# Kernel optimization log

Hardware: AMD Instinct MI355X
Metric: run time of the kernel (lower is better)

## Reference

```python
import jax, jax.numpy as jnp
import numpy as np

N_S = 4096      # number of sentences
N_K = 8192      # number of knowledge entries
HID = 1024      # settings.hidden_dim
SENT = 1024     # settings.sent_dim


def setup_inputs() -> dict:
    key = jax.random.key(0)
    ks = jax.random.split(key, 6)
    sentences = jax.random.normal(ks[0], (N_S, SENT), dtype=jnp.float32)
    knowledge = jax.random.normal(ks[1], (N_K, 3 * HID), dtype=jnp.float32)
    # Linear params stored as [in, out] for x @ W + b
    Ws = jax.random.normal(ks[2], (SENT, HID), dtype=jnp.float32) * 0.02
    bs = jnp.zeros((HID,), dtype=jnp.float32)
    Wk = jax.random.normal(ks[3], (3 * HID, HID), dtype=jnp.float32) * 0.02
    bk = jnp.zeros((HID,), dtype=jnp.float32)
    return {"sentences": sentences, "knowledge": knowledge,
            "Ws": Ws, "bs": bs, "Wk": Wk, "bk": bk}


def reference(sentences, knowledge, Ws, bs, Wk, bk):
    S = sentences @ Ws + bs                  # [N_s, h]
    K = knowledge @ Wk + bk                  # [N_k, h]
    align_scores = S @ K.T                   # [N_s, N_k]
    # NOTE: softmax over dim=0 (sentence axis), exactly as the torch module
    attentions = jax.nn.softmax(align_scores, axis=0)
    fused = attentions @ knowledge           # [N_s, 3h]
    return (fused, attentions)
```

## Files before the change

### kernel.cpp

```cpp
#include <hip/hip_runtime.h>
#include <hip/hip_bf16.h>
#include <cstdint>
#include <cstddef>

#define N_S 4096
#define N_Kn 8192
#define HID 1024
#define SENT 1024
#define K3 3072

typedef __attribute__((ext_vector_type(4))) float f4;
typedef __attribute__((ext_vector_type(8))) short bf8;
typedef __attribute__((ext_vector_type(4))) short bf4;
typedef unsigned short u16;

__device__ __forceinline__ u16 f2bf(float x) {
    __hip_bfloat16 h = __float2bfloat16(x);
    return __builtin_bit_cast(u16, h);
}
__device__ __forceinline__ float bf2f(u16 u) {
    union { unsigned int u; float f; } v; v.u = ((unsigned int)u) << 16;
    return v.f;
}

__device__ __forceinline__ void gl16(const u16* g, u16* l) {
    __builtin_amdgcn_global_load_lds(
        (const __attribute__((address_space(1))) void*)g,
        (__attribute__((address_space(3))) void*)l, 16, 0, 0);
}

__device__ __forceinline__ int xcd_swz(int bid, int nwg) {
    const int cpx = nwg >> 3;
    return (bid & 7) * cpx + (bid >> 3);
}

__global__ __launch_bounds__(256) void transpose_split_f32(
    const float* __restrict__ in, u16* __restrict__ hi, u16* __restrict__ lo,
    int R, int C)
{
    __shared__ float tile[32][33];
    const int bx = blockIdx.x * 32, by = blockIdx.y * 32;
    const int tx = threadIdx.x & 31, ty = threadIdx.x >> 5;
#pragma unroll
    for (int i = 0; i < 32; i += 8)
        tile[ty + i][tx] = in[(size_t)(by + ty + i) * C + bx + tx];
    __syncthreads();
#pragma unroll
    for (int i = 0; i < 32; i += 8) {
        const float v = tile[tx][ty + i];
        const u16 h = f2bf(v);
        const size_t o = (size_t)(bx + ty + i) * R + by + tx;
        hi[o] = h;
        lo[o] = f2bf(v - bf2f(h));
    }
}

__global__ __launch_bounds__(256) void transpose_f32_bf16(
    const float* __restrict__ in, u16* __restrict__ out, int R, int C)
{
    __shared__ float tile[32][33];
    const int bx = blockIdx.x * 32, by = blockIdx.y * 32;
    const int tx = threadIdx.x & 31, ty = threadIdx.x >> 5;
#pragma unroll
    for (int i = 0; i < 32; i += 8)
        tile[ty + i][tx] = in[(size_t)(by + ty + i) * C + bx + tx];
    __syncthreads();
#pragma unroll
    for (int i = 0; i < 32; i += 8)
        out[(size_t)(bx + ty + i) * R + by + tx] = f2bf(tile[tx][ty + i]);
}

#define G8_LDA(buf, mh) \
  _Pragma("unroll") for (int m_ = 0; m_ < 4; ++m_) \
  _Pragma("unroll") for (int kk_ = 0; kk_ < 2; ++kk_) \
    fa[m_][kk_] = *(const bf8*)&sA[buf][wm][((mh)*64 + m_*16 + fr)*64 + (((kk_*4+kg) ^ (fr&7))<<3)];

#define G8_LDB(buf, nh, FB) \
  _Pragma("unroll") for (int nn_ = 0; nn_ < 2; ++nn_) \
  _Pragma("unroll") for (int kk_ = 0; kk_ < 2; ++kk_) \
    FB[nn_][kk_] = *(const bf8*)&sB[buf][hb][(cb + (nh)*32 + nn_*16 + fr)*64 + (((kk_*4+kg) ^ (fr&7))<<3)];

#define G8_MMA(mh, nh, FB) \
  _Pragma("unroll") for (int kk_ = 0; kk_ < 2; ++kk_) \
  _Pragma("unroll") for (int m_ = 0; m_ < 4; ++m_) \
  _Pragma("unroll") for (int nn_ = 0; nn_ < 2; ++nn_) \
    acc[(mh)*4+m_][(nh)*2+nn_] = __builtin_amdgcn_mfma_f32_16x16x32_bf16( \
        fa[m_][kk_], FB[nn_][kk_], acc[(mh)*4+m_][(nh)*2+nn_], 0, 0, 0);

#define BARR __builtin_amdgcn_s_barrier()
#define PRIO1 __builtin_amdgcn_s_setprio(1)
#define PRIO0 __builtin_amdgcn_s_setprio(0)
#define VM8  asm volatile("s_waitcnt vmcnt(8)" ::: "memory")
#define VM0  asm volatile("s_waitcnt vmcnt(0)" ::: "memory")

__global__ __launch_bounds__(512, 2) void gemm8(
    const u16* __restrict__ A, const u16* __restrict__ B,
    float* __restrict__ C, int N, int Kd, int gx)
{
    __shared__ u16 sA[2][2][8192];
    __shared__ u16 sB[2][2][8192];

    const int swz = xcd_swz(blockIdx.x, gridDim.x);
    const int bx = swz % gx, by = swz / gx;
    const long brow = (long)by * 256, bcol = (long)bx * 256;

    const int t = threadIdx.x;
    const int w = t >> 6, l = t & 63;
    const int fr = l & 15, kg = l >> 4;
    const int wm = w >> 2;
    const int wn = w & 3;
    const int hb = wn >> 1;
    const int cb = (wn & 1) * 64;

    const int srow = t >> 3;
    const int schk = ((t & 7) ^ (srow & 7)) << 3;
    const int sldb = w << 9;

    auto stA = [&](int buf, int h, int kt) {
        const u16* g = A + (brow + h * 128 + srow) * (long)Kd + ((long)kt << 6) + schk;
        gl16(g, &sA[buf][h][sldb]);
        gl16(g + 64 * (long)Kd, &sA[buf][h][4096 + sldb]);
    };
    auto stB = [&](int buf, int h, int kt) {
        const u16* g = B + (bcol + h * 128 + srow) * (long)Kd + ((long)kt << 6) + schk;
        gl16(g, &sB[buf][h][sldb]);
        gl16(g + 64 * (long)Kd, &sB[buf][h][4096 + sldb]);
    };

    f4 acc[8][4];
#pragma unroll
    for (int m = 0; m < 8; ++m)
#pragma unroll
        for (int n = 0; n < 4; ++n) acc[m][n] = (f4){0.f, 0.f, 0.f, 0.f};

    bf8 fa[4][2], fb0[2][2], fb1[2][2];

    const int NK = Kd >> 6;

    stB(0, 0, 0); stB(0, 1, 0); stA(0, 0, 0); stA(0, 1, 0);
    stB(1, 0, 1); stB(1, 1, 1); stA(1, 0, 1); stA(1, 1, 1);
    VM8;
    BARR;

    for (int it = 0; it < (NK >> 1); ++it) {
        const int t2 = 2 * it + 2, t3 = 2 * it + 3;
        const bool s2 = t2 < NK, s3 = t3 < NK;

        G8_LDA(0, 0); G8_LDB(0, 0, fb0);
        BARR; PRIO1; G8_MMA(0, 0, fb0); PRIO0; BARR;
        G8_LDB(0, 1, fb1);
        BARR; PRIO1; G8_MMA(0, 1, fb1); PRIO0; BARR;
        G8_LDA(0, 1);
        if (s2) { stB(0, 0, t2); stB(0, 1, t2); }
        BARR; PRIO1; G8_MMA(1, 0, fb0); PRIO0; BARR;
        if (s2) { stA(0, 0, t2); stA(0, 1, t2); }
        BARR; PRIO1; G8_MMA(1, 1, fb1); PRIO0;
        if (s2) { VM8; } else { VM0; }
        BARR;

        G8_LDA(1, 0); G8_LDB(1, 0, fb0);
        BARR; PRIO1; G8_MMA(0, 0, fb0); PRIO0; BARR;
        G8_LDB(1, 1, fb1);
        BARR; PRIO1; G8_MMA(0, 1, fb1); PRIO0; BARR;
        G8_LDA(1, 1);
        if (s3) { stB(1, 0, t3); stB(1, 1, t3); }
        BARR; PRIO1; G8_MMA(1, 0, fb0); PRIO0; BARR;
        if (s3) { stA(1, 0, t3); stA(1, 1, t3); }
        BARR; PRIO1; G8_MMA(1, 1, fb1); PRIO0;
        if (s3) { VM8; } else { VM0; }
        BARR;
    }

#pragma unroll
    for (int n = 0; n < 4; ++n) {
        const long c = bcol + wn * 64 + n * 16 + fr;
#pragma unroll
        for (int m = 0; m < 8; ++m) {
            const long r0 = brow + wm * 128 + m * 16 + kg * 4;
#pragma unroll
            for (int r = 0; r < 4; ++r)
                C[(r0 + r) * (long)N + c] = acc[m][n][r];
        }
    }
}

template <bool SPLIT, bool AF32, bool EPIS>
__global__ __launch_bounds__(256) void gemm_mfma(
    const void* __restrict__ Aany, const u16* __restrict__ Alo_,
    const u16* __restrict__ Bhi_, const u16* __restrict__ Blo_,
    float* __restrict__ Cf, u16* __restrict__ Chi, u16* __restrict__ Clo,
    const float* __restrict__ bias, int N, int Kd, int gx)
{
    constexpr int SA = AF32 ? 48 : 32;
    __shared__ u16 sAh[128 * SA];
    __shared__ u16 sAl[SPLIT ? 128 * SA : 8];
    __shared__ u16 sBh[128 * 32];
    __shared__ u16 sBl[SPLIT ? 128 * 32 : 8];

    const int swz = xcd_swz(blockIdx.x, gridDim.x);
    const int nst_x = gx >> 2;
    const int st = swz >> 4, off = swz & 15;
    const int bxi = (st % nst_x) * 4 + (off & 3);
    const int byi = (st / nst_x) * 4 + (off >> 2);

    const int t = threadIdx.x;
    const int w = t >> 6;
    const int l = t & 63;
    const long brow = (long)byi * 128;
    const long bcol = (long)bxi * 128;

    const int grow = l >> 2;
    const int gcol = ((l & 3) ^ ((l >> 3) & 3)) * 8;

    const int wr = (w >> 1) * 64;
    const int wc = (w & 1) * 64;
    const int fr = l & 15;
    const int kg = l >> 4;
    const int kq = (kg ^ ((fr >> 1) & 3)) * 8;

    f4 acc[4][4];
#pragma unroll
    for (int m = 0; m < 4; m++)
#pragma unroll
        for (int n = 0; n < 4; n++) acc[m][n] = (f4){0.f, 0.f, 0.f, 0.f};

    const int nkt = Kd >> 5;
    for (int kt = 0; kt < nkt; ++kt) {
        const int k0 = kt * 32;

#pragma unroll
        for (int i = 0; i < 2; ++i) {
            const long r = bcol + i * 64 + w * 16 + grow;
            const int lb = i * 2048 + w * 512;
            gl16(Bhi_ + r * Kd + k0 + gcol, sBh + lb);
            if constexpr (SPLIT) gl16(Blo_ + r * Kd + k0 + gcol, sBl + lb);
        }

        if constexpr (!AF32) {
            const u16* Ahi = (const u16*)Aany;
#pragma unroll
            for (int i = 0; i < 2; ++i) {
                const long r = brow + i * 64 + w * 16 + grow;
                const int lb = i * 2048 + w * 512;
                gl16(Ahi + r * Kd + k0 + gcol, sAh + lb);
                if constexpr (SPLIT) gl16(Alo_ + r * Kd + k0 + gcol, sAl + lb);
            }
        } else {
            const float* Af = (const float*)Aany;
            const int ar = w * 8 + (l >> 3);
            const int cF = (l & 7) * 4;
#pragma unroll
            for (int j = 0; j < 4; ++j) {
                const int r = j * 32 + ar;
                const f4 v = *(const f4*)(Af + (brow + r) * (long)Kd + k0 + cF);
                u16 h[4], lw[4];
#pragma unroll
                for (int q = 0; q < 4; ++q) {
                    h[q] = f2bf(v[q]);
                    if constexpr (SPLIT) lw[q] = f2bf(v[q] - bf2f(h[q]));
                }
                *(bf4*)&sAh[r * SA + cF] = *(bf4*)h;
                if constexpr (SPLIT) *(bf4*)&sAl[r * SA + cF] = *(bf4*)lw;
            }
        }
        __syncthreads();

        bf8 fah[4], fbh[4], fal[4], fbl[4];
#pragma unroll
        for (int m = 0; m < 4; ++m) {
            if constexpr (AF32) {
                fah[m] = *(bf8*)&sAh[(wr + m * 16 + fr) * SA + kg * 8];
                if constexpr (SPLIT) fal[m] = *(bf8*)&sAl[(wr + m * 16 + fr) * SA + kg * 8];
            } else {
                fah[m] = *(bf8*)&sAh[(wr + m * 16 + fr) * 32 + kq];
                if constexpr (SPLIT) fal[m] = *(bf8*)&sAl[(wr + m * 16 + fr) * 32 + kq];
            }
            fbh[m] = *(bf8*)&sBh[(wc + m * 16 + fr) * 32 + kq];
            if constexpr (SPLIT) fbl[m] = *(bf8*)&sBl[(wc + m * 16 + fr) * 32 + kq];
        }
#pragma unroll
        for (int m = 0; m < 4; ++m)
#pragma unroll
            for (int n = 0; n < 4; ++n) {
                acc[m][n] = __builtin_amdgcn_mfma_f32_16x16x32_bf16(fah[m], fbh[n], acc[m][n], 0, 0, 0);
                if constexpr (SPLIT) {
                    acc[m][n] = __builtin_amdgcn_mfma_f32_16x16x32_bf16(fah[m], fbl[n], acc[m][n], 0, 0, 0);
                    acc[m][n] = __builtin_amdgcn_mfma_f32_16x16x32_bf16(fal[m], fbh[n], acc[m][n], 0, 0, 0);
                }
            }
        __syncthreads();
    }

#pragma unroll
    for (int n = 0; n < 4; ++n) {
        const long c = bcol + wc + n * 16 + fr;
        float bv = 0.f;
        if constexpr (EPIS) bv = bias[c];
#pragma unroll
        for (int m = 0; m < 4; ++m) {
            const long r0 = brow + wr + m * 16 + kg * 4;
#pragma unroll
            for (int r = 0; r < 4; ++r) {
                const float v = acc[m][n][r] + bv;
                if constexpr (EPIS) {
                    const u16 h = f2bf(v);
                    Chi[(r0 + r) * (long)N + c] = h;
                    Clo[(r0 + r) * (long)N + c] = f2bf(v - bf2f(h));
                } else {
                    Cf[(r0 + r) * (long)N + c] = v;
                }
            }
        }
    }
}

#define RCHUNK 128

__global__ __launch_bounds__(256) void softmax_partial(
    const float* __restrict__ align, float* __restrict__ pm, float* __restrict__ ps)
{
    const int col = blockIdx.x * 256 + threadIdx.x;
    const int r0 = blockIdx.y * RCHUNK;
    float m = -3.4e38f;
    for (int r = 0; r < RCHUNK; r++)
        m = fmaxf(m, align[(size_t)(r0 + r) * N_Kn + col]);
    float s = 0.f;
    for (int r = 0; r < RCHUNK; r++)
        s += __expf(align[(size_t)(r0 + r) * N_Kn + col] - m);
    pm[(size_t)blockIdx.y * N_Kn + col] = m;
    ps[(size_t)blockIdx.y * N_Kn + col] = s;
}

__global__ __launch_bounds__(256) void softmax_combine(
    const float* __restrict__ pm, const float* __restrict__ ps,
    float* __restrict__ fm, float* __restrict__ fsinv)
{
    const int col = blockIdx.x * 256 + threadIdx.x;
    float m = -3.4e38f;
#pragma unroll
    for (int i = 0; i < 32; i++) m = fmaxf(m, pm[(size_t)i * N_Kn + col]);
    float s = 0.f;
#pragma unroll
    for (int i = 0; i < 32; i++)
        s += ps[(size_t)i * N_Kn + col] * __expf(pm[(size_t)i * N_Kn + col] - m);
    fm[col] = m;
    fsinv[col] = 1.f / s;
}

__global__ __launch_bounds__(256) void softmax_norm(
    float* __restrict__ align, u16* __restrict__ abf,
    const float* __restrict__ fm, const float* __restrict__ fsinv)
{
    const int col = blockIdx.x * 256 + threadIdx.x;
    const int r0 = blockIdx.y * RCHUNK;
    const float m = fm[col], si = fsinv[col];
    for (int r = 0; r < RCHUNK; r++) {
        const size_t idx = (size_t)(r0 + r) * N_Kn + col;
        const float v = __expf(align[idx] - m) * si;
        align[idx] = v;
        abf[idx] = f2bf(v);
    }
}

extern "C" void kernel_launch(void* const* d_in, const int* in_sizes, int n_in,
                              void* d_out, int out_size, void* d_ws, size_t ws_size,
                              hipStream_t stream)
{
    const float* sentences = (const float*)d_in[0];
    const float* knowledge = (const float*)d_in[1];
    const float* Ws = (const float*)d_in[2];
    const float* bs = (const float*)d_in[3];
    const float* Wk = (const float*)d_in[4];
    const float* bk = (const float*)d_in[5];

    float* out_fused = (float*)d_out;
    float* out_attn = (float*)d_out + (size_t)N_S * K3;

    char* w = (char*)d_ws;
    u16* attn_bf = (u16*)w;
    u16* WsT_hi = (u16*)w; w += (size_t)HID * SENT * 2;
    u16* WsT_lo = (u16*)w; w += (size_t)HID * SENT * 2;
    u16* WkT_hi = (u16*)w; w += (size_t)HID * K3 * 2;
    u16* WkT_lo = (u16*)w; w += (size_t)HID * K3 * 2;
    u16* S_hi   = (u16*)w; w += (size_t)N_S * HID * 2;
    u16* S_lo   = (u16*)w; w += (size_t)N_S * HID * 2;
    u16* K_hi   = (u16*)w; w += (size_t)N_Kn * HID * 2;
    u16* K_lo   = (u16*)w; w += (size_t)N_Kn * HID * 2;
    u16* kT     = (u16*)w; w += (size_t)K3 * N_Kn * 2;
    float* pm   = (float*)w; w += (size_t)32 * N_Kn * 4;
    float* ps   = (float*)w; w += (size_t)32 * N_Kn * 4;
    float* fm   = (float*)w; w += (size_t)N_Kn * 4;
    float* fsv  = (float*)w; w += (size_t)N_Kn * 4;

    transpose_split_f32<<<dim3(HID / 32, SENT / 32), 256, 0, stream>>>(Ws, WsT_hi, WsT_lo, SENT, HID);
    transpose_split_f32<<<dim3(HID / 32, K3 / 32), 256, 0, stream>>>(Wk, WkT_hi, WkT_lo, K3, HID);
    transpose_f32_bf16<<<dim3(K3 / 32, N_Kn / 32), 256, 0, stream>>>(knowledge, kT, N_Kn, K3);

    gemm_mfma<true, true, true><<<(HID / 128) * (N_S / 128), 256, 0, stream>>>(
        sentences, nullptr, WsT_hi, WsT_lo, nullptr, S_hi, S_lo, bs, HID, SENT, HID / 128);

    gemm_mfma<true, true, true><<<(HID / 128) * (N_Kn / 128), 256, 0, stream>>>(
        knowledge, nullptr, WkT_hi, WkT_lo, nullptr, K_hi, K_lo, bk, HID, K3, HID / 128);

    gemm_mfma<true, false, false><<<(N_Kn / 128) * (N_S / 128), 256, 0, stream>>>(
        S_hi, S_lo, K_hi, K_lo, out_attn, nullptr, nullptr, nullptr, N_Kn, HID, N_Kn / 128);

    softmax_partial<<<dim3(N_Kn / 256, N_S / RCHUNK), 256, 0, stream>>>(out_attn, pm, ps);
    softmax_combine<<<dim3(N_Kn / 256), 256, 0, stream>>>(pm, ps, fm, fsv);
    softmax_norm<<<dim3(N_Kn / 256, N_S / RCHUNK), 256, 0, stream>>>(out_attn, attn_bf, fm, fsv);

    gemm8<<<(K3 / 256) * (N_S / 256), 512, 0, stream>>>(
        attn_bf, kT, out_fused, K3, N_Kn, K3 / 256);
}
```

Baseline: 783.5 us.

## Retile final attention-knowledge GEMM to 256x192 blocks for full CU occupancy

Replaces the 256x256-tile GEMM for attn @ knowledge with a 256x192-tile variant using a 4x2 wave layout of 64x96 sub-tiles and a single-step double-buffered K loop with prefetched B fragments. The grid grows from 192 to 256 blocks, which should fill all compute units instead of leaving some idle. In exchange, per-block data reuse is lower and the pipeline schedule and wait counts are rewritten, so there is a risk of less latency hiding.

```diff
diff --git a/kernel.cpp b/kernel.cpp
--- a/kernel.cpp
+++ b/kernel.cpp
@@ -70,113 +70,106 @@
         out[(size_t)(bx + ty + i) * R + by + tx] = f2bf(tile[tx][ty + i]);
 }
 
-#define G8_LDA(buf, mh) \
-  _Pragma("unroll") for (int m_ = 0; m_ < 4; ++m_) \
-  _Pragma("unroll") for (int kk_ = 0; kk_ < 2; ++kk_) \
-    fa[m_][kk_] = *(const bf8*)&sA[buf][wm][((mh)*64 + m_*16 + fr)*64 + (((kk_*4+kg) ^ (fr&7))<<3)];
-
-#define G8_LDB(buf, nh, FB) \
-  _Pragma("unroll") for (int nn_ = 0; nn_ < 2; ++nn_) \
-  _Pragma("unroll") for (int kk_ = 0; kk_ < 2; ++kk_) \
-    FB[nn_][kk_] = *(const bf8*)&sB[buf][hb][(cb + (nh)*32 + nn_*16 + fr)*64 + (((kk_*4+kg) ^ (fr&7))<<3)];
-
-#define G8_MMA(mh, nh, FB) \
-  _Pragma("unroll") for (int kk_ = 0; kk_ < 2; ++kk_) \
-  _Pragma("unroll") for (int m_ = 0; m_ < 4; ++m_) \
-  _Pragma("unroll") for (int nn_ = 0; nn_ < 2; ++nn_) \
-    acc[(mh)*4+m_][(nh)*2+nn_] = __builtin_amdgcn_mfma_f32_16x16x32_bf16( \
-        fa[m_][kk_], FB[nn_][kk_], acc[(mh)*4+m_][(nh)*2+nn_], 0, 0, 0);
-
 #define BARR __builtin_amdgcn_s_barrier()
 #define PRIO1 __builtin_amdgcn_s_setprio(1)
 #define PRIO0 __builtin_amdgcn_s_setprio(0)
-#define VM8  asm volatile("s_waitcnt vmcnt(8)" ::: "memory")
+#define VM7  asm volatile("s_waitcnt vmcnt(7)" ::: "memory")
 #define VM0  asm volatile("s_waitcnt vmcnt(0)" ::: "memory")
 
-__global__ __launch_bounds__(512, 2) void gemm8(
+#define GB_LDA(buf, mh) \
+  _Pragma("unroll") for (int mf_ = 0; mf_ < 2; ++mf_) \
+  _Pragma("unroll") for (int kk_ = 0; kk_ < 2; ++kk_) \
+    fa[mf_][kk_] = *(const bf8*)&sA[buf][(wm*64 + ((mh)*2+mf_)*16 + fr)*64 + (((kk_*4+kg) ^ (fr&7))<<3)];
+
+#define GB_LDB(buf, nh, FB) \
+  _Pragma("unroll") for (int nf_ = 0; nf_ < 3; ++nf_) \
+  _Pragma("unroll") for (int kk_ = 0; kk_ < 2; ++kk_) \
+    FB[nf_][kk_] = *(const bf8*)&sB[buf][(wn*96 + ((nh)*3+nf_)*16 + fr)*64 + (((kk_*4+kg) ^ (fr&7))<<3)];
+
+#define GB_MMA(mh, nh, FB) \
+  _Pragma("unroll") for (int kk_ = 0; kk_ < 2; ++kk_) \
+  _Pragma("unroll") for (int mf_ = 0; mf_ < 2; ++mf_) \
+  _Pragma("unroll") for (int nf_ = 0; nf_ < 3; ++nf_) \
+    acc[(mh)*2+mf_][(nh)*3+nf_] = __builtin_amdgcn_mfma_f32_16x16x32_bf16( \
+        fa[mf_][kk_], FB[nf_][kk_], acc[(mh)*2+mf_][(nh)*3+nf_], 0, 0, 0);
+
+__global__ __launch_bounds__(512, 2) void gemm8b(
     const u16* __restrict__ A, const u16* __restrict__ B,
     float* __restrict__ C, int N, int Kd, int gx)
 {
-    __shared__ u16 sA[2][2][8192];
-    __shared__ u16 sB[2][2][8192];
+    __shared__ u16 sA[2][256 * 64];
+    __shared__ u16 sB[2][192 * 64];
 
     const int swz = xcd_swz(blockIdx.x, gridDim.x);
     const int bx = swz % gx, by = swz / gx;
-    const long brow = (long)by * 256, bcol = (long)bx * 256;
+    const long brow = (long)by * 256, bcol = (long)bx * 192;
 
     const int t = threadIdx.x;
     const int w = t >> 6, l = t & 63;
     const int fr = l & 15, kg = l >> 4;
-    const int wm = w >> 2;
-    const int wn = w & 3;
-    const int hb = wn >> 1;
-    const int cb = (wn & 1) * 64;
+    const int wm = w >> 1;
+    const int wn = w & 1;
 
     const int srow = t >> 3;
     const int schk = ((t & 7) ^ (srow & 7)) << 3;
     const int sldb = w << 9;
 
-    auto stA = [&](int buf, int h, int kt) {
-        const u16* g = A + (brow + h * 128 + srow) * (long)Kd + ((long)kt << 6) + schk;
-        gl16(g, &sA[buf][h][sldb]);
-        gl16(g + 64 * (long)Kd, &sA[buf][h][4096 + sldb]);
+    auto stA = [&](int buf, int s, int kt) {
+        gl16(A + (brow + s * 64 + srow) * (long)Kd + ((long)kt << 6) + schk,
+             &sA[buf][s * 4096 + sldb]);
     };
-    auto stB = [&](int buf, int h, int kt) {
-        const u16* g = B + (bcol + h * 128 + srow) * (long)Kd + ((long)kt << 6) + schk;
-        gl16(g, &sB[buf][h][sldb]);
-        gl16(g + 64 * (long)Kd, &sB[buf][h][4096 + sldb]);
+    auto stB = [&](int buf, int s, int kt) {
+        gl16(B + (bcol + s * 64 + srow) * (long)Kd + ((long)kt << 6) + schk,
+             &sB[buf][s * 4096 + sldb]);
     };
 
-    f4 acc[8][4];
-#pragma unroll
-    for (int m = 0; m < 8; ++m)
-#pragma unroll
-        for (int n = 0; n < 4; ++n) acc[m][n] = (f4){0.f, 0.f, 0.f, 0.f};
-
-    bf8 fa[4][2], fb0[2][2], fb1[2][2];
+    f4 acc[4][6];
+#pragma unroll
+    for (int m = 0; m < 4; ++m)
+#pragma unroll
+        for (int n = 0; n < 6; ++n) acc[m][n] = (f4){0.f, 0.f, 0.f, 0.f};
+
+    bf8 fa[2][2], fb0[3][2], fb1[3][2];
 
     const int NK = Kd >> 6;
 
-    stB(0, 0, 0); stB(0, 1, 0); stA(0, 0, 0); stA(0, 1, 0);
-    stB(1, 0, 1); stB(1, 1, 1); stA(1, 0, 1); stA(1, 1, 1);
-    VM8;
+    stB(0, 0, 0); stB(0, 1, 0); stB(0, 2, 0);
+    stA(0, 0, 0); stA(0, 1, 0); stA(0, 2, 0); stA(0, 3, 0);
+    stB(1, 0, 1); stB(1, 1, 1); stB(1, 2, 1);
+    stA(1, 0, 1); stA(1, 1, 1); stA(1, 2, 1); stA(1, 3, 1);
+    VM7;
     BARR;
-
-    for (int it = 0; it < (NK >> 1); ++it) {
-        const int t2 = 2 * it + 2, t3 = 2 * it + 3;
-        const bool s2 = t2 < NK, s3 = t3 < NK;
-
-        G8_LDA(0, 0); G8_LDB(0, 0, fb0);
-        BARR; PRIO1; G8_MMA(0, 0, fb0); PRIO0; BARR;
-        G8_LDB(0, 1, fb1);
-        BARR; PRIO1; G8_MMA(0, 1, fb1); PRIO0; BARR;
-        G8_LDA(0, 1);
-        if (s2) { stB(0, 0, t2); stB(0, 1, t2); }
-        BARR; PRIO1; G8_MMA(1, 0, fb0); PRIO0; BARR;
-        if (s2) { stA(0, 0, t2); stA(0, 1, t2); }
-        BARR; PRIO1; G8_MMA(1, 1, fb1); PRIO0;
-        if (s2) { VM8; } else { VM0; }
+    GB_LDB(0, 0, fb0);
+
+    for (int kt = 0; kt < NK; ++kt) {
+        const int buf = kt & 1;
+        const int t2 = kt + 2;
+        const bool s2 = t2 < NK;
+
+        GB_LDA(buf, 0);
+        BARR; PRIO1; GB_MMA(0, 0, fb0); PRIO0; BARR;
+
+        GB_LDB(buf, 1, fb1);
+        if (s2) { stB(buf, 0, t2); stB(buf, 1, t2); stB(buf, 2, t2); }
+        BARR; PRIO1; GB_MMA(0, 1, fb1); PRIO0; BARR;
+
+        GB_LDA(buf, 1);
+        if (s2) { stA(buf, 0, t2); stA(buf, 1, t2); stA(buf, 2, t2); stA(buf, 3, t2); }
+        BARR; PRIO1; GB_MMA(1, 0, fb0); PRIO0; BARR;
+
+        if (s2) { VM7; } else { VM0; }
         BARR;
-
-        G8_LDA(1, 0); G8_LDB(1, 0, fb0);
-        BARR; PRIO1; G8_MMA(0, 0, fb0); PRIO0; BARR;
-        G8_LDB(1, 1, fb1);
-        BARR; PRIO1; G8_MMA(0, 1, fb1); PRIO0; BARR;
-        G8_LDA(1, 1);
-        if (s3) { stB(1, 0, t3); stB(1, 1, t3); }
-        BARR; PRIO1; G8_MMA(1, 0, fb0); PRIO0; BARR;
-        if (s3) { stA(1, 0, t3); stA(1, 1, t3); }
-        BARR; PRIO1; G8_MMA(1, 1, fb1); PRIO0;
-        if (s3) { VM8; } else { VM0; }
+        GB_LDB(buf ^ 1, 0, fb0);
+        PRIO1; GB_MMA(1, 1, fb1); PRIO0;
         BARR;
     }
 
 #pragma unroll
-    for (int n = 0; n < 4; ++n) {
-        const long c = bcol + wn * 64 + n * 16 + fr;
-#pragma unroll
-        for (int m = 0; m < 8; ++m) {
-            const long r0 = brow + wm * 128 + m * 16 + kg * 4;
+    for (int n = 0; n < 6; ++n) {
+        const long c = bcol + wn * 96 + n * 16 + fr;
+#pragma unroll
+        for (int m = 0; m < 4; ++m) {
+            const long r0 = brow + wm * 64 + m * 16 + kg * 4;
 #pragma unroll
             for (int r = 0; r < 4; ++r)
                 C[(r0 + r) * (long)N + c] = acc[m][n][r];
@@ -409,6 +402,6 @@
     softmax_combine<<<dim3(N_Kn / 256), 256, 0, stream>>>(pm, ps, fm, fsv);
     softmax_norm<<<dim3(N_Kn / 256, N_S / RCHUNK), 256, 0, stream>>>(out_attn, attn_bf, fm, fsv);
 
-    gemm8<<<(K3 / 256) * (N_S / 256), 512, 0, stream>>>(
-        attn_bf, kT, out_fused, K3, N_Kn, K3 / 256);
-}
+    gemm8b<<<(K3 / 192) * (N_S / 256), 512, 0, stream>>>(
+        attn_bf, kT, out_fused, K3, N_Kn, K3 / 192);
+}
```

Result: no change. 785.1 us (+0.2%).
